# Kernel tuning notes

Hardware: AMD Instinct MI355X
Metric: run time of the kernel (lower is better)

The kernel has to match this reference:

```python
import jax, jax.numpy as jnp
import numpy as np

NEG_BIG = -1.0e9


def setup_inputs() -> dict:
    key = jax.random.key(0)
    kq, kk, kv, km = jax.random.split(key, 4)
    B, H, S, D = 8, 16, 1024, 64
    q = jax.random.normal(kq, (B, H, S, D), dtype=jnp.float32)
    k = jax.random.normal(kk, (B, H, S, D), dtype=jnp.float32)
    v = jax.random.normal(kv, (B, H, S, D), dtype=jnp.float32)
    mask = jax.random.uniform(km, (S - 1, S - 1), dtype=jnp.float32)
    return {"q": q, "k": k, "v": v, "mask": mask}


def reference(q, k, v, mask):
    # scores: [B,H,S,S]
    dk = k.shape[-1]
    logits = jnp.einsum("bhsd,bhtd->bhst", q, k) / jnp.sqrt(jnp.asarray(dk, q.dtype))
    if mask is not None:
        # original adds mask*-1e9 only on logits[:, :, 1:, 1:];
        # equivalent to padding mask with a zero first row/col then adding.
        mask_padded = jnp.pad(mask, ((1, 0), (1, 0)))  # [S, S]
        logits = logits + mask_padded * NEG_BIG
    attention_weights = jax.nn.softmax(logits, axis=-1)
    output = jnp.einsum("bhst,bhtd->bhsd", attention_weights, v)
    return (output, attention_weights)
```

## Files before the change

kernel.cpp:

```cpp
#include <hip/hip_runtime.h>

#define S_LEN 1024
#define D_DIM 64
#define QB 16
#define NTHREADS 1024
#define LSTR 1036
#define ESTR 2072
#define ELO 1024
#define RINV_OFF 66304
#define SC_OFF 66368
#define LDS_BYTES 78656

#define NBH 128
#define KV_ELEMS ((size_t)NBH * S_LEN * D_DIM)
#define WS_NEED (KV_ELEMS * 8)

typedef short s16x8 __attribute__((ext_vector_type(8)));
typedef short s16x4 __attribute__((ext_vector_type(4)));
typedef float f32x4 __attribute__((ext_vector_type(4)));
typedef unsigned short u16;
typedef unsigned int u32;

static __device__ __forceinline__ float bf2f(u16 h) {
  return __builtin_bit_cast(float, ((u32)h) << 16);
}

static __device__ __forceinline__ u16 f2bf_rne(float f) {
  u32 u = __builtin_bit_cast(u32, f);
  return (u16)((u + 0x7fffu + ((u >> 16) & 1u)) >> 16);
}

static __device__ __forceinline__ void split2(float f, u16& h, u16& l) {
  u32 u = __builtin_bit_cast(u32, f);
  h = (u16)(u >> 16);
  float hf = __builtin_bit_cast(float, u & 0xffff0000u);
  l = f2bf_rne(f - hf);
}

static __device__ __forceinline__ f32x4 mfma16(s16x8 a, s16x8 b, f32x4 c) {
  return __builtin_amdgcn_mfma_f32_16x16x32_bf16(a, b, c, 0, 0, 0);
}

static __device__ __forceinline__ void cvt8(f32x4 a, f32x4 b, s16x8& h, s16x8& l) {
  s16x8 hh, ll;
#pragma unroll
  for (int j = 0; j < 8; ++j) {
    float fj = (j < 4) ? a[j] : b[j - 4];
    u16 hb, lb;
    split2(fj, hb, lb);
    hh[j] = (short)hb;
    ll[j] = (short)lb;
  }
  h = hh; l = ll;
}

extern "C" __global__ void __launch_bounds__(256)
presplit_k(const float* __restrict__ kg, u16* __restrict__ khi, u16* __restrict__ klo) {
  const size_t base = ((size_t)blockIdx.x * 256 + threadIdx.x) * 8;
  f32x4 a = __builtin_nontemporal_load((const f32x4*)(kg + base));
  f32x4 b = __builtin_nontemporal_load((const f32x4*)(kg + base + 4));
  s16x8 h, l;
  cvt8(a, b, h, l);
  *(s16x8*)(khi + base) = h;
  *(s16x8*)(klo + base) = l;
}

extern "C" __global__ void __launch_bounds__(256)
presplit_vt(const float* __restrict__ vg, u16* __restrict__ vthi, u16* __restrict__ vtlo) {
  __shared__ u16 ht[64][72];
  __shared__ u16 lt[64][72];
  const int tid = threadIdx.x;
  const int bh = blockIdx.x >> 4;
  const int t0 = (blockIdx.x & 15) * 64;
  const float* vp = vg + ((size_t)bh * S_LEN + t0) * D_DIM;
#pragma unroll
  for (int it = 0; it < 16; ++it) {
    const int idx = it * 256 + tid;
    float f = __builtin_nontemporal_load(vp + idx);
    u16 h, l;
    split2(f, h, l);
    ht[idx & 63][idx >> 6] = h;
    lt[idx & 63][idx >> 6] = l;
  }
  __syncthreads();
#pragma unroll
  for (int o = tid; o < 2048; o += 256) {
    const int d = o >> 5;
    const int tp = (o & 31) * 2;
    u32 wh = (u32)ht[d][tp] | ((u32)ht[d][tp + 1] << 16);
    u32 wl = (u32)lt[d][tp] | ((u32)lt[d][tp + 1] << 16);
    const size_t off = ((size_t)bh * D_DIM + d) * S_LEN + t0 + tp;
    *(u32*)(vthi + off) = wh;
    *(u32*)(vtlo + off) = wl;
  }
}

template <bool PRE>
__global__ __launch_bounds__(NTHREADS, 8) void
attn_fused(const float* __restrict__ qg, const float* __restrict__ kg,
           const float* __restrict__ vg, const float* __restrict__ mg,
           float* __restrict__ og, float* __restrict__ wg,
           const u16* __restrict__ khi, const u16* __restrict__ klo,
           const u16* __restrict__ vthi, const u16* __restrict__ vtlo)
{
  extern __shared__ char smem[];
  float* L = (float*)smem;
  u16* E = (u16*)smem;
  float* rinv = (float*)(smem + RINV_OFF);
  float* sc = (float*)(smem + SC_OFF);

  const int tid = threadIdx.x;
  const int wave = tid >> 6;
  const int lane = tid & 63;
  const int l15 = lane & 15;
  const int lg4 = lane >> 4;

  const int bid = (int)blockIdx.x;
  const int swz = (bid & 7) * 1024 + (bid >> 3);
  const int qb = swz & 63;
  const int bh = swz >> 6;
  const int qbase = qb * QB;

  const float* qp = qg + (size_t)bh * S_LEN * D_DIM;

  {
    s16x8 qh[2], ql[2];
    const float* qrow = qp + (size_t)(qbase + l15) * D_DIM + lg4 * 8;
#pragma unroll
    for (int ks = 0; ks < 2; ++ks) {
      f32x4 a = *(const f32x4*)(qrow + ks * 32);
      f32x4 b = *(const f32x4*)(qrow + ks * 32 + 4);
#pragma unroll
      for (int j = 0; j < 4; ++j) { a[j] *= 0.125f; b[j] *= 0.125f; }
      cvt8(a, b, qh[ks], ql[ks]);
    }

#pragma unroll 2
    for (int ct = 0; ct < 4; ++ct) {
      const int t = wave * 64 + ct * 16 + l15;
      s16x8 kh[2], kl[2];
      if constexpr (PRE) {
        const u16* kb = khi + ((size_t)bh * S_LEN + t) * D_DIM + lg4 * 8;
        const u16* lb = klo + ((size_t)bh * S_LEN + t) * D_DIM + lg4 * 8;
#pragma unroll
        for (int ks = 0; ks < 2; ++ks) {
          kh[ks] = *(const s16x8*)(kb + ks * 32);
          kl[ks] = *(const s16x8*)(lb + ks * 32);
        }
      } else {
        const float* krow = kg + ((size_t)bh * S_LEN + t) * D_DIM + lg4 * 8;
#pragma unroll
        for (int ks = 0; ks < 2; ++ks) {
          f32x4 a = *(const f32x4*)(krow + ks * 32);
          f32x4 b = *(const f32x4*)(krow + ks * 32 + 4);
          cvt8(a, b, kh[ks], kl[ks]);
        }
      }
      f32x4 acc = {0.f, 0.f, 0.f, 0.f};
#pragma unroll
      for (int ks = 0; ks < 2; ++ks) {
        acc = mfma16(qh[ks], kh[ks], acc);
        acc = mfma16(qh[ks], kl[ks], acc);
        acc = mfma16(ql[ks], kh[ks], acc);
      }
#pragma unroll
      for (int j = 0; j < 4; ++j) {
        const int rl = lg4 * 4 + j;
        const int s = qbase + rl;
        float mv = 0.f;
        if (s > 0 && t > 0) mv = mg[(size_t)(s - 1) * (S_LEN - 1) + (t - 1)];
        L[rl * LSTR + t] = fmaf(mv, -1.0e9f, acc[j]);
      }
    }
  }
  __syncthreads();

  {
    const float* Lr = L + wave * LSTR;
    f32x4 lv[4];
#pragma unroll
    for (int g = 0; g < 4; ++g) lv[g] = *(const f32x4*)&Lr[lane * 4 + g * 256];
    float m = -3.402823466e38f;
#pragma unroll
    for (int g = 0; g < 4; ++g)
#pragma unroll
      for (int j = 0; j < 4; ++j) m = fmaxf(m, lv[g][j]);
#pragma unroll
    for (int off = 1; off < 64; off <<= 1) m = fmaxf(m, __shfl_xor(m, off, 64));

    float sum = 0.f;
#pragma unroll
    for (int g = 0; g < 4; ++g)
#pragma unroll
      for (int j = 0; j < 4; ++j) {
        float ex = __expf(lv[g][j] - m);
        lv[g][j] = ex;
        sum += ex;
      }
#pragma unroll
    for (int off = 1; off < 64; off <<= 1) sum += __shfl_xor(sum, off, 64);
    const float inv = 1.0f / sum;
    if (lane == 0) rinv[wave] = inv;

    u16* Er = E + wave * ESTR;
#pragma unroll
    for (int g = 0; g < 4; ++g) {
      const int col = lane * 4 + g * 256;
      s16x4 eh, el;
#pragma unroll
      for (int j = 0; j < 4; ++j) {
        u16 hb, lb;
        split2(lv[g][j], hb, lb);
        eh[j] = (short)hb;
        el[j] = (short)lb;
      }
      *(s16x4*)&Er[col] = eh;
      *(s16x4*)&Er[ELO + col] = el;
    }
  }
  __syncthreads();

  const int g3 = wave >> 2;
  const int ct = wave & 3;
  const int dcol = ct * 16 + l15;
  f32x4 acc = {0.f, 0.f, 0.f, 0.f};
#pragma unroll 2
  for (int T = g3 * 8; T < g3 * 8 + 8; ++T) {
    const int t0 = T * 32 + lg4 * 8;
    s16x8 vh, vl;
    if constexpr (PRE) {
      const size_t off = ((size_t)bh * D_DIM + dcol) * S_LEN + t0;
      vh = *(const s16x8*)(vthi + off);
      vl = *(const s16x8*)(vtlo + off);
    } else {
#pragma unroll
      for (int i = 0; i < 8; ++i) {
        u16 hb, lb;
        split2(vg[((size_t)bh * S_LEN + t0 + i) * D_DIM + dcol], hb, lb);
        vh[i] = (short)hb;
        vl[i] = (short)lb;
      }
    }
    s16x8 ah = *(const s16x8*)&E[l15 * ESTR + t0];
    s16x8 al = *(const s16x8*)&E[l15 * ESTR + ELO + t0];
    acc = mfma16(ah, vh, acc);
    acc = mfma16(ah, vl, acc);
    acc = mfma16(al, vh, acc);
  }

  if (g3 > 0) {
#pragma unroll
    for (int j = 0; j < 4; ++j)
      sc[(g3 - 1) * 1024 + (lg4 * 4 + j) * 64 + dcol] = acc[j];
  }
  __syncthreads();

  if (g3 == 0) {
    float* op = og + (size_t)bh * S_LEN * D_DIM;
#pragma unroll
    for (int j = 0; j < 4; ++j) {
      const int rl = lg4 * 4 + j;
      float s = acc[j] + sc[rl * 64 + dcol] + sc[1024 + rl * 64 + dcol] +
                sc[2048 + rl * 64 + dcol];
      __builtin_nontemporal_store(s * rinv[rl],
          &op[(size_t)(qbase + rl) * D_DIM + dcol]);
    }
  }

  {
    const float winv = rinv[wave];
    const u16* Er = E + wave * ESTR;
    float* wrow = wg + (size_t)bh * S_LEN * S_LEN + (size_t)(qbase + wave) * S_LEN;
#pragma unroll
    for (int g = 0; g < 4; ++g) {
      const int col = lane * 4 + g * 256;
      s16x4 eh = *(const s16x4*)&Er[col];
      s16x4 el = *(const s16x4*)&Er[ELO + col];
      f32x4 wv;
#pragma unroll
      for (int j = 0; j < 4; ++j)
        wv[j] = (bf2f((u16)eh[j]) + bf2f((u16)el[j])) * winv;
      __builtin_nontemporal_store(wv, (f32x4*)&wrow[col]);
    }
  }
}

extern "C" void kernel_launch(void* const* d_in, const int* in_sizes, int n_in,
                              void* d_out, int out_size, void* d_ws, size_t ws_size,
                              hipStream_t stream) {
  const float* q = (const float*)d_in[0];
  const float* k = (const float*)d_in[1];
  const float* v = (const float*)d_in[2];
  const float* m = (const float*)d_in[3];
  float* out = (float*)d_out;
  float* w = out + (size_t)8 * 16 * S_LEN * D_DIM;

  u16* khi = (u16*)d_ws;
  u16* klo = khi + KV_ELEMS;
  u16* vthi = klo + KV_ELEMS;
  u16* vtlo = vthi + KV_ELEMS;

  if (ws_size >= WS_NEED) {
    presplit_k<<<dim3(4096), 256, 0, stream>>>(k, khi, klo);
    presplit_vt<<<dim3(2048), 256, 0, stream>>>(v, vthi, vtlo);
    hipFuncSetAttribute(reinterpret_cast<const void*>(attn_fused<true>),
                        hipFuncAttributeMaxDynamicSharedMemorySize, LDS_BYTES);
    attn_fused<true><<<dim3(8192), NTHREADS, LDS_BYTES, stream>>>(
        q, k, v, m, out, w, khi, klo, vthi, vtlo);
  } else {
    hipFuncSetAttribute(reinterpret_cast<const void*>(attn_fused<false>),
                        hipFuncAttributeMaxDynamicSharedMemorySize, LDS_BYTES);
    attn_fused<false><<<dim3(8192), NTHREADS, LDS_BYTES, stream>>>(
        q, k, v, m, out, w, khi, klo, vthi, vtlo);
  }
}
```

Measured before the change: 1.134 ms.

## Move mask add into softmax pass with vector loads; write weights early

The mask is no longer loaded as scattered scalars inside the QK^T MFMA loop. It is now read row-wise with unaligned float4 loads in the softmax stage, where each wave owns one row. Attention weights are written straight from the fp32 exp values during softmax instead of after the PV stage, which drops the bf16 hi/lo reconstruction pass. Nontemporal loads and stores are replaced with plain ones. The weight stores can now overlap the PV compute, at the cost of more register pressure in the softmax section.

```diff
diff --git a/kernel.cpp b/kernel.cpp
--- a/kernel.cpp
+++ b/kernel.cpp
@@ -18,12 +18,9 @@
 typedef short s16x8 __attribute__((ext_vector_type(8)));
 typedef short s16x4 __attribute__((ext_vector_type(4)));
 typedef float f32x4 __attribute__((ext_vector_type(4)));
+typedef float f32x4u __attribute__((ext_vector_type(4), aligned(4)));
 typedef unsigned short u16;
 typedef unsigned int u32;
-
-static __device__ __forceinline__ float bf2f(u16 h) {
-  return __builtin_bit_cast(float, ((u32)h) << 16);
-}
 
 static __device__ __forceinline__ u16 f2bf_rne(float f) {
   u32 u = __builtin_bit_cast(u32, f);
@@ -57,8 +54,8 @@
 extern "C" __global__ void __launch_bounds__(256)
 presplit_k(const float* __restrict__ kg, u16* __restrict__ khi, u16* __restrict__ klo) {
   const size_t base = ((size_t)blockIdx.x * 256 + threadIdx.x) * 8;
-  f32x4 a = __builtin_nontemporal_load((const f32x4*)(kg + base));
-  f32x4 b = __builtin_nontemporal_load((const f32x4*)(kg + base + 4));
+  f32x4 a = *(const f32x4*)(kg + base);
+  f32x4 b = *(const f32x4*)(kg + base + 4);
   s16x8 h, l;
   cvt8(a, b, h, l);
   *(s16x8*)(khi + base) = h;
@@ -76,7 +73,7 @@
 #pragma unroll
   for (int it = 0; it < 16; ++it) {
     const int idx = it * 256 + tid;
-    float f = __builtin_nontemporal_load(vp + idx);
+    float f = vp[idx];
     u16 h, l;
     split2(f, h, l);
     ht[idx & 63][idx >> 6] = h;
@@ -164,22 +161,41 @@
         acc = mfma16(ql[ks], kh[ks], acc);
       }
 #pragma unroll
-      for (int j = 0; j < 4; ++j) {
-        const int rl = lg4 * 4 + j;
-        const int s = qbase + rl;
-        float mv = 0.f;
-        if (s > 0 && t > 0) mv = mg[(size_t)(s - 1) * (S_LEN - 1) + (t - 1)];
-        L[rl * LSTR + t] = fmaf(mv, -1.0e9f, acc[j]);
-      }
+      for (int j = 0; j < 4; ++j)
+        L[(lg4 * 4 + j) * LSTR + t] = acc[j];
     }
   }
   __syncthreads();
 
   {
+    const int s = qbase + wave;
     const float* Lr = L + wave * LSTR;
     f32x4 lv[4];
 #pragma unroll
     for (int g = 0; g < 4; ++g) lv[g] = *(const f32x4*)&Lr[lane * 4 + g * 256];
+
+    if (s > 0) {
+      const float* mrow = mg + (size_t)(s - 1) * (S_LEN - 1);
+      if (lane == 0) {
+        lv[0][1] = fmaf(mrow[0], -1.0e9f, lv[0][1]);
+        lv[0][2] = fmaf(mrow[1], -1.0e9f, lv[0][2]);
+        lv[0][3] = fmaf(mrow[2], -1.0e9f, lv[0][3]);
+#pragma unroll
+        for (int g = 1; g < 4; ++g) {
+          f32x4 mv = *(const f32x4u*)(mrow + g * 256 - 1);
+#pragma unroll
+          for (int j = 0; j < 4; ++j) lv[g][j] = fmaf(mv[j], -1.0e9f, lv[g][j]);
+        }
+      } else {
+#pragma unroll
+        for (int g = 0; g < 4; ++g) {
+          f32x4 mv = *(const f32x4u*)(mrow + lane * 4 + g * 256 - 1);
+#pragma unroll
+          for (int j = 0; j < 4; ++j) lv[g][j] = fmaf(mv[j], -1.0e9f, lv[g][j]);
+        }
+      }
+    }
+
     float m = -3.402823466e38f;
 #pragma unroll
     for (int g = 0; g < 4; ++g)
@@ -202,18 +218,22 @@
     const float inv = 1.0f / sum;
     if (lane == 0) rinv[wave] = inv;
 
+    float* wrow = wg + (size_t)bh * S_LEN * S_LEN + (size_t)(qbase + wave) * S_LEN;
     u16* Er = E + wave * ESTR;
 #pragma unroll
     for (int g = 0; g < 4; ++g) {
       const int col = lane * 4 + g * 256;
+      f32x4 wv;
       s16x4 eh, el;
 #pragma unroll
       for (int j = 0; j < 4; ++j) {
+        wv[j] = lv[g][j] * inv;
         u16 hb, lb;
         split2(lv[g][j], hb, lb);
         eh[j] = (short)hb;
         el[j] = (short)lb;
       }
+      *(f32x4*)&wrow[col] = wv;
       *(s16x4*)&Er[col] = eh;
       *(s16x4*)&Er[ELO + col] = el;
     }
@@ -262,25 +282,7 @@
       const int rl = lg4 * 4 + j;
       float s = acc[j] + sc[rl * 64 + dcol] + sc[1024 + rl * 64 + dcol] +
                 sc[2048 + rl * 64 + dcol];
-      __builtin_nontemporal_store(s * rinv[rl],
-          &op[(size_t)(qbase + rl) * D_DIM + dcol]);
-    }
-  }
-
-  {
-    const float winv = rinv[wave];
-    const u16* Er = E + wave * ESTR;
-    float* wrow = wg + (size_t)bh * S_LEN * S_LEN + (size_t)(qbase + wave) * S_LEN;
-#pragma unroll
-    for (int g = 0; g < 4; ++g) {
-      const int col = lane * 4 + g * 256;
-      s16x4 eh = *(const s16x4*)&Er[col];
-      s16x4 el = *(const s16x4*)&Er[ELO + col];
-      f32x4 wv;
-#pragma unroll
-      for (int j = 0; j < 4; ++j)
-        wv[j] = (bf2f((u16)eh[j]) + bf2f((u16)el[j])) * winv;
-      __builtin_nontemporal_store(wv, (f32x4*)&wrow[col]);
+      op[(size_t)(qbase + rl) * D_DIM + dcol] = s * rinv[rl];
     }
   }
 }
```

Result: no change. 1.115 ms (-1.6%).
